# Kernel optimization log

Hardware: AMD Instinct MI355X
Metric: run time of the kernel (lower is better)

## Reference

```python
import jax, jax.numpy as jnp
import numpy as np

D_MODEL = 1024
N_HEADS = 16
D_K = D_MODEL // N_HEADS
D_FF = 4096
EPS = 1e-5


def _layernorm(x, g, b):
    mu = jnp.mean(x, axis=-1, keepdims=True)
    var = jnp.var(x, axis=-1, keepdims=True)
    return (x - mu) * jax.lax.rsqrt(var + EPS) * g + b


def setup_inputs() -> dict:
    key = jax.random.key(0)
    ks = jax.random.split(key, 12)
    s = 0.02
    x = jax.random.normal(ks[0], (2, 2048, D_MODEL), dtype=jnp.float32)
    # Linear weights stored [in, out] so y = x @ W + b
    wq = jax.random.normal(ks[1], (D_MODEL, D_MODEL), dtype=jnp.float32) * s
    wk = jax.random.normal(ks[2], (D_MODEL, D_MODEL), dtype=jnp.float32) * s
    wv = jax.random.normal(ks[3], (D_MODEL, D_MODEL), dtype=jnp.float32) * s
    wo = jax.random.normal(ks[4], (D_MODEL, D_MODEL), dtype=jnp.float32) * s
    bq = jnp.zeros((D_MODEL,), jnp.float32)
    bk = jnp.zeros((D_MODEL,), jnp.float32)
    bv = jnp.zeros((D_MODEL,), jnp.float32)
    bo = jnp.zeros((D_MODEL,), jnp.float32)
    ln1_g = jnp.ones((D_MODEL,), jnp.float32)
    ln1_b = jnp.zeros((D_MODEL,), jnp.float32)
    ln2_g = jnp.ones((D_MODEL,), jnp.float32)
    ln2_b = jnp.zeros((D_MODEL,), jnp.float32)
    w1 = jax.random.normal(ks[5], (D_MODEL, D_FF), dtype=jnp.float32) * s
    b1 = jnp.zeros((D_FF,), jnp.float32)
    w2 = jax.random.normal(ks[6], (D_FF, D_MODEL), dtype=jnp.float32) * s
    b2 = jnp.zeros((D_MODEL,), jnp.float32)
    return {"x": x, "wq": wq, "bq": bq, "wk": wk, "bk": bk, "wv": wv, "bv": bv,
            "wo": wo, "bo": bo, "ln1_g": ln1_g, "ln1_b": ln1_b,
            "ln2_g": ln2_g, "ln2_b": ln2_b, "w1": w1, "b1": b1, "w2": w2, "b2": b2}


def reference(x, wq, bq, wk, bk, wv, bv, wo, bo, ln1_g, ln1_b, ln2_g, ln2_b, w1, b1, w2, b2):
    B, S, _ = x.shape
    res = x
    # project and split heads: [B, S, H, Dk]
    q = (x @ wq + bq).reshape(B, S, N_HEADS, D_K)
    k = (x @ wk + bk).reshape(B, S, N_HEADS, D_K)
    v = (x @ wv + bv).reshape(B, S, N_HEADS, D_K)
    # full score matrix [B, H, Sq, Sk] (faithful to unfused original)
    scores = jnp.einsum('bqhd,bkhd->bhqk', q, k) / jnp.sqrt(jnp.float32(D_K))
    weights = jax.nn.softmax(scores, axis=-1)
    attn = jnp.einsum('bhqk,bkhd->bqhd', weights, v).reshape(B, S, D_MODEL)
    x = _layernorm(res + attn @ wo + bo, ln1_g, ln1_b)
    res = x
    h = jax.nn.relu(x @ w1 + b1)
    x = _layernorm(res + h @ w2 + b2, ln2_g, ln2_b)
    return x
```

## Files before the change

kernel.cpp:

```cpp
#include <hip/hip_runtime.h>
#include <hip/hip_bf16.h>
#include <stdint.h>


typedef __hip_bfloat16 bf16;
typedef short bf16x8 __attribute__((ext_vector_type(8)));
typedef float f32x4 __attribute__((ext_vector_type(4)));

__device__ __forceinline__ float bf2f_lo(unsigned u) { return __uint_as_float(u << 16); }
__device__ __forceinline__ float bf2f_hi(unsigned u) { return __uint_as_float(u & 0xffff0000u); }
__device__ __forceinline__ ushort f2bf(float f) {
  union { bf16 h; ushort u; } c; c.h = __float2bfloat16(f); return c.u;
}
__device__ __forceinline__ bool is_f32(const uint* probe) { return probe[0] == 0x3F800000u; }
__device__ __forceinline__ float ld_param(const void* p, size_t i, bool f32) {
  return f32 ? ((const float*)p)[i] : __bfloat162float(((const bf16*)p)[i]);
}

template <bool A_EXT, bool RES_EXT>
__device__ __forceinline__ void gemm_body(
    const void* __restrict__ Av, const ushort* __restrict__ BT,
    const void* __restrict__ bias, const void* __restrict__ res,
    void* __restrict__ C, int N_, int K_, int bm, int bn,
    int kb, int ke, int mode, const uint* probe) {
  __shared__ ushort Asm_[128 * 32];
  __shared__ ushort Bsm_[128 * 32];

  const bool F32 = is_f32(probe);
  const bool AF = A_EXT && F32;

  const int tid = threadIdx.x;
  const int wave = tid >> 6;
  const int lane = tid & 63;
  const int wm = wave & 1, wn = wave >> 1;

  const int r0 = tid >> 2;
  const int c0 = (tid & 3) * 8;
  const int dA0 = r0 * 32 + c0;
  const int dA1 = dA0 + 64 * 32;

  const size_t aRow0 = (size_t)(bm * 128 + r0) * K_;
  const size_t aRow1 = aRow0 + (size_t)64 * K_;
  const ushort* pB0 = BT + (size_t)(bn * 128 + r0) * K_ + c0;
  const ushort* pB1 = pB0 + (size_t)64 * K_;

  auto ld4 = [&](int kk, uint4& A0, uint4& A1, uint4& B0, uint4& B1) {
    if (AF) {
      const float* Af = (const float*)Av;
      const float4 f0 = *(const float4*)(Af + aRow0 + kk + c0);
      const float4 f1 = *(const float4*)(Af + aRow0 + kk + c0 + 4);
      const float4 g0 = *(const float4*)(Af + aRow1 + kk + c0);
      const float4 g1 = *(const float4*)(Af + aRow1 + kk + c0 + 4);
      A0.x = (uint)f2bf(f0.x) | ((uint)f2bf(f0.y) << 16);
      A0.y = (uint)f2bf(f0.z) | ((uint)f2bf(f0.w) << 16);
      A0.z = (uint)f2bf(f1.x) | ((uint)f2bf(f1.y) << 16);
      A0.w = (uint)f2bf(f1.z) | ((uint)f2bf(f1.w) << 16);
      A1.x = (uint)f2bf(g0.x) | ((uint)f2bf(g0.y) << 16);
      A1.y = (uint)f2bf(g0.z) | ((uint)f2bf(g0.w) << 16);
      A1.z = (uint)f2bf(g1.x) | ((uint)f2bf(g1.y) << 16);
      A1.w = (uint)f2bf(g1.z) | ((uint)f2bf(g1.w) << 16);
    } else {
      const ushort* Ab = (const ushort*)Av;
      A0 = *(const uint4*)(Ab + aRow0 + kk + c0);
      A1 = *(const uint4*)(Ab + aRow1 + kk + c0);
    }
    B0 = *(const uint4*)(pB0 + kk);
    B1 = *(const uint4*)(pB1 + kk);
  };

  f32x4 zero = {0.f, 0.f, 0.f, 0.f};
  f32x4 acc[4][4];
#pragma unroll
  for (int i = 0; i < 4; ++i)
#pragma unroll
    for (int j = 0; j < 4; ++j) acc[i][j] = zero;

  const int m16 = lane & 15;
  const int quad = lane >> 4;
  const int koff = quad * 8;

  uint4 a0, a1, b0, b1;
  ld4(kb, a0, a1, b0, b1);

  for (int k0 = kb; k0 < ke; k0 += 32) {
    __syncthreads();
    *(uint4*)&Asm_[dA0] = a0;
    *(uint4*)&Asm_[dA1] = a1;
    *(uint4*)&Bsm_[dA0] = b0;
    *(uint4*)&Bsm_[dA1] = b1;
    __syncthreads();

    if (k0 + 32 < ke) ld4(k0 + 32, a0, a1, b0, b1);

    bf16x8 af[4], bfr[4];
#pragma unroll
    for (int i = 0; i < 4; ++i)
      af[i] = *(const bf16x8*)&Asm_[(wm * 64 + i * 16 + m16) * 32 + koff];
#pragma unroll
    for (int j = 0; j < 4; ++j)
      bfr[j] = *(const bf16x8*)&Bsm_[(wn * 64 + j * 16 + m16) * 32 + koff];
#pragma unroll
    for (int i = 0; i < 4; ++i)
#pragma unroll
      for (int j = 0; j < 4; ++j)
        acc[i][j] = __builtin_amdgcn_mfma_f32_16x16x32_bf16(af[i], bfr[j], acc[i][j], 0, 0, 0);
  }

  const int row0 = bm * 128 + wm * 64;
  const int col0 = bn * 128 + wn * 64;
#pragma unroll
  for (int j = 0; j < 4; ++j) {
    const int col = col0 + j * 16 + m16;
    const float bv = (mode == 3) ? 0.f : ld_param(bias, col, F32);
#pragma unroll
    for (int i = 0; i < 4; ++i) {
#pragma unroll
      for (int r = 0; r < 4; ++r) {
        const int row = row0 + i * 16 + quad * 4 + r;
        float v = acc[i][j][r] + bv;
        if (mode == 1) v = fmaxf(v, 0.f);
        if (mode == 2) v += ld_param(res, (size_t)row * N_ + col, RES_EXT && F32);
        if (mode >= 2) ((float*)C)[(size_t)row * N_ + col] = v;
        else ((bf16*)C)[(size_t)row * N_ + col] = __float2bfloat16(v);
      }
    }
  }
}

__global__ __launch_bounds__(256) void gemm_qkv(
    const void* A, const ushort* BT0, const ushort* BT1, const ushort* BT2,
    const void* b0, const void* b1, const void* b2,
    bf16* C0, bf16* C1, bf16* C2, const uint* probe) {
  const int sel = blockIdx.y >> 3, bn = blockIdx.y & 7;
  const ushort* BT = sel == 0 ? BT0 : (sel == 1 ? BT1 : BT2);
  const void* bb = sel == 0 ? b0 : (sel == 1 ? b1 : b2);
  bf16* C = sel == 0 ? C0 : (sel == 1 ? C1 : C2);
  gemm_body<true, false>(A, BT, bb, nullptr, C, 1024, 1024, blockIdx.x, bn,
                         0, 1024, 0, probe);
}
__global__ __launch_bounds__(256) void gemm_wo_sk(
    const ushort* A, const ushort* BT, const void* bias, const void* res,
    float* C0, float* C1, const uint* probe) {
  const int kz = blockIdx.z;
  gemm_body<false, true>(A, BT, bias, res, kz ? C1 : C0, 1024, 1024,
                         blockIdx.x, blockIdx.y, kz * 512, kz * 512 + 512,
                         kz ? 3 : 2, probe);
}
__global__ __launch_bounds__(256) void gemm_ffn1(
    const ushort* A, const ushort* BT, const void* bias, bf16* C, const uint* probe) {
  gemm_body<false, false>(A, BT, bias, nullptr, C, 4096, 1024,
                          blockIdx.x, blockIdx.y, 0, 1024, 1, probe);
}
__global__ __launch_bounds__(256) void gemm_ffn2_sk(
    const ushort* A, const ushort* BT, const void* bias, const ushort* res,
    float* C0, float* C1, const uint* probe) {
  const int kz = blockIdx.z;
  gemm_body<false, false>(A, BT, bias, res, kz ? C1 : C0, 1024, 4096,
                          blockIdx.x, blockIdx.y, kz * 2048, kz * 2048 + 2048,
                          kz ? 3 : 2, probe);
}

__global__ __launch_bounds__(256) void transpose_all(
    const void* W0, const void* W1, const void* W2, const void* W3,
    const void* W4, const void* W5,
    ushort* D0, ushort* D1, ushort* D2, ushort* D3, ushort* D4, ushort* D5,
    const uint* probe) {
  const int z = blockIdx.z;
  if (z < 4 && blockIdx.x >= 32) return;
  int n0, k0, K_, N_;
  const void* W;
  ushort* D;
  if (z < 4) {
    n0 = blockIdx.x * 32; k0 = blockIdx.y * 32; K_ = 1024; N_ = 1024;
    W = z == 0 ? W0 : z == 1 ? W1 : z == 2 ? W2 : W3;
    D = z == 0 ? D0 : z == 1 ? D1 : z == 2 ? D2 : D3;
  } else if (z == 4) {
    n0 = blockIdx.x * 32; k0 = blockIdx.y * 32; K_ = 1024; N_ = 4096; W = W4; D = D4;
  } else {
    n0 = blockIdx.y * 32; k0 = blockIdx.x * 32; K_ = 4096; N_ = 1024; W = W5; D = D5;
  }
  const bool F32 = is_f32(probe);
  __shared__ ushort tile[32][33];
  const int tx = threadIdx.x & 31, ty = threadIdx.x >> 5;
#pragma unroll
  for (int i = 0; i < 32; i += 8) {
    const size_t src = (size_t)(k0 + ty + i) * N_ + n0 + tx;
    tile[ty + i][tx] = F32 ? f2bf(((const float*)W)[src]) : ((const ushort*)W)[src];
  }
  __syncthreads();
#pragma unroll
  for (int i = 0; i < 32; i += 8)
    D[(size_t)(n0 + ty + i) * K_ + k0 + tx] = tile[tx][ty + i];
}

template <bool OUT_EXT>
__global__ __launch_bounds__(256) void ln_kernel(
    const float* __restrict__ X, const float* __restrict__ P,
    const void* __restrict__ g, const void* __restrict__ bta,
    void* __restrict__ out, const uint* probe) {
  const bool F32 = is_f32(probe);
  const int row = blockIdx.x;
  const int tid = threadIdx.x;
  const float4 a = *(const float4*)(X + (size_t)row * 1024 + tid * 4);
  const float4 b = *(const float4*)(P + (size_t)row * 1024 + tid * 4);
  const float xv[4] = {a.x + b.x, a.y + b.y, a.z + b.z, a.w + b.w};
  float s = xv[0] + xv[1] + xv[2] + xv[3];
  float ss = xv[0] * xv[0] + xv[1] * xv[1] + xv[2] * xv[2] + xv[3] * xv[3];
#pragma unroll
  for (int o = 32; o > 0; o >>= 1) { s += __shfl_down(s, o); ss += __shfl_down(ss, o); }
  __shared__ float red[8];
  if ((tid & 63) == 0) { red[tid >> 6] = s; red[4 + (tid >> 6)] = ss; }
  __syncthreads();
  s = red[0] + red[1] + red[2] + red[3];
  ss = red[4] + red[5] + red[6] + red[7];
  const float mu = s * (1.f / 1024.f);
  const float rstd = rsqrtf(ss * (1.f / 1024.f) - mu * mu + 1e-5f);
#pragma unroll
  for (int i = 0; i < 4; ++i) {
    const size_t idx = (size_t)row * 1024 + tid * 4 + i;
    const float y = (xv[i] - mu) * rstd * ld_param(g, tid * 4 + i, F32) +
                    ld_param(bta, tid * 4 + i, F32);
    if (OUT_EXT && F32) ((float*)out)[idx] = y;
    else ((bf16*)out)[idx] = __float2bfloat16(y);
  }
}

__global__ __launch_bounds__(256) void attn_mfma(
    const ushort* __restrict__ Qm, const ushort* __restrict__ Km,
    const ushort* __restrict__ Vm, ushort* __restrict__ Om) {
  __shared__ ushort Ks[64 * 72];
  __shared__ ushort Vt[64 * 72];
  __shared__ ushort Pw[4][32 * 72];

  const int tid = threadIdx.x;
  const int wave = tid >> 6, lane = tid & 63;
  const int m16 = lane & 15, quad = lane >> 4;
  const int bb = blockIdx.z, h = blockIdx.y;
  const size_t hb = ((size_t)bb * 2048) * 1024 + h * 64;
  const int q0 = blockIdx.x * 128 + wave * 32;

  bf16x8 qf[2][2];
#pragma unroll
  for (int i = 0; i < 2; ++i)
#pragma unroll
    for (int c = 0; c < 2; ++c) {
      const uint4 u = *(const uint4*)(Qm + hb + (size_t)(q0 + 16 * i + m16) * 1024 + c * 32 + quad * 8);
      const uint w[4] = {u.x, u.y, u.z, u.w};
      bf16x8 f;
#pragma unroll
      for (int j = 0; j < 4; ++j) {
        f[2 * j]     = (short)f2bf(bf2f_lo(w[j]) * 0.125f);
        f[2 * j + 1] = (short)f2bf(bf2f_hi(w[j]) * 0.125f);
      }
      qf[i][c] = f;
    }

  f32x4 zero = {0.f, 0.f, 0.f, 0.f};
  f32x4 acc[2][4];
#pragma unroll
  for (int i = 0; i < 2; ++i)
#pragma unroll
    for (int j = 0; j < 4; ++j) acc[i][j] = zero;
  float lp[2][4] = {{0.f, 0.f, 0.f, 0.f}, {0.f, 0.f, 0.f, 0.f}};

  const int skey = tid >> 2;
  const int sd = (tid & 3) * 8;
  const int pp = tid & 31;
  const int dc = tid >> 5;
  const int ka_ = 16 * ((2 * pp) & 3) + ((2 * pp) >> 2);
  const int kb_ = 16 * ((2 * pp + 1) & 3) + ((2 * pp + 1) >> 2);
  const ushort* Kg = Km + hb;
  const ushort* Vg = Vm + hb;

  uint4 kr0, kr1, vr0, vr1;
  kr0 = *(const uint4*)(Kg + (size_t)skey * 1024 + sd);
  kr1 = *(const uint4*)(Kg + (size_t)skey * 1024 + sd + 32);
  vr0 = *(const uint4*)(Vg + (size_t)ka_ * 1024 + dc * 8);
  vr1 = *(const uint4*)(Vg + (size_t)kb_ * 1024 + dc * 8);

  for (int kt = 0; kt < 2048; kt += 64) {
    __syncthreads();
    *(uint4*)&Ks[skey * 72 + sd] = kr0;
    *(uint4*)&Ks[skey * 72 + sd + 32] = kr1;
    {
      const uint va[4] = {vr0.x, vr0.y, vr0.z, vr0.w};
      const uint vb[4] = {vr1.x, vr1.y, vr1.z, vr1.w};
#pragma unroll
      for (int j = 0; j < 8; ++j) {
        const uint lo = (j & 1) ? (va[j >> 1] >> 16) : (va[j >> 1] & 0xffffu);
        const uint hi = (j & 1) ? (vb[j >> 1] & 0xffff0000u) : (vb[j >> 1] << 16);
        *(uint*)&Vt[(dc * 8 + j) * 72 + 2 * pp] = lo | hi;
      }
    }
    __syncthreads();

    if (kt + 64 < 2048) {
      kr0 = *(const uint4*)(Kg + (size_t)(kt + 64 + skey) * 1024 + sd);
      kr1 = *(const uint4*)(Kg + (size_t)(kt + 64 + skey) * 1024 + sd + 32);
      vr0 = *(const uint4*)(Vg + (size_t)(kt + 64 + ka_) * 1024 + dc * 8);
      vr1 = *(const uint4*)(Vg + (size_t)(kt + 64 + kb_) * 1024 + dc * 8);
    }

    f32x4 s[2][4];
#pragma unroll
    for (int i = 0; i < 2; ++i)
#pragma unroll
      for (int jn = 0; jn < 4; ++jn) s[i][jn] = zero;
#pragma unroll
    for (int c = 0; c < 2; ++c) {
      bf16x8 kb4[4];
#pragma unroll
      for (int jn = 0; jn < 4; ++jn)
        kb4[jn] = *(const bf16x8*)&Ks[(jn * 16 + m16) * 72 + c * 32 + quad * 8];
#pragma unroll
      for (int i = 0; i < 2; ++i)
#pragma unroll
        for (int jn = 0; jn < 4; ++jn)
          s[i][jn] = __builtin_amdgcn_mfma_f32_16x16x32_bf16(qf[i][c], kb4[jn], s[i][jn], 0, 0, 0);
    }

#pragma unroll
    for (int i = 0; i < 2; ++i)
#pragma unroll
      for (int r = 0; r < 4; ++r) {
        const float p0 = __expf(s[i][0][r]);
        const float p1 = __expf(s[i][1][r]);
        const float p2 = __expf(s[i][2][r]);
        const float p3 = __expf(s[i][3][r]);
        lp[i][r] += (p0 + p1) + (p2 + p3);
        uint2 pk;
        pk.x = (uint)f2bf(p0) | ((uint)f2bf(p1) << 16);
        pk.y = (uint)f2bf(p2) | ((uint)f2bf(p3) << 16);
        *(uint2*)&Pw[wave][(16 * i + quad * 4 + r) * 72 + m16 * 4] = pk;
      }
    asm volatile("s_waitcnt lgkmcnt(0)" ::: "memory");

#pragma unroll
    for (int c = 0; c < 2; ++c) {
      bf16x8 pa[2], vb4[4];
#pragma unroll
      for (int i = 0; i < 2; ++i)
        pa[i] = *(const bf16x8*)&Pw[wave][(16 * i + m16) * 72 + c * 32 + quad * 8];
#pragma unroll
      for (int jd = 0; jd < 4; ++jd)
        vb4[jd] = *(const bf16x8*)&Vt[(jd * 16 + m16) * 72 + c * 32 + quad * 8];
#pragma unroll
      for (int i = 0; i < 2; ++i)
#pragma unroll
        for (int jd = 0; jd < 4; ++jd)
          acc[i][jd] = __builtin_amdgcn_mfma_f32_16x16x32_bf16(pa[i], vb4[jd], acc[i][jd], 0, 0, 0);
    }
  }

#pragma unroll
  for (int i = 0; i < 2; ++i)
#pragma unroll
    for (int r = 0; r < 4; ++r) {
      float l = lp[i][r];
      l += __shfl_xor(l, 1); l += __shfl_xor(l, 2);
      l += __shfl_xor(l, 4); l += __shfl_xor(l, 8);
      const float inv = 1.f / l;
      const size_t rowoff = hb + (size_t)(q0 + 16 * i + quad * 4 + r) * 1024;
#pragma unroll
      for (int jd = 0; jd < 4; ++jd)
        Om[rowoff + jd * 16 + m16] = f2bf(acc[i][jd][r] * inv);
    }
}

extern "C" void kernel_launch(void* const* d_in, const int* in_sizes, int n_in,
                              void* d_out, int out_size, void* d_ws, size_t ws_size,
                              hipStream_t stream) {
  const void* x   = d_in[0];
  const void* wq  = d_in[1];
  const void* bq  = d_in[2];
  const void* wk  = d_in[3];
  const void* bk  = d_in[4];
  const void* wv  = d_in[5];
  const void* bv  = d_in[6];
  const void* wo  = d_in[7];
  const void* bo  = d_in[8];
  const uint* probe = (const uint*)d_in[9];
  const void* ln1g = d_in[9];
  const void* ln1b = d_in[10];
  const void* ln2g = d_in[11];
  const void* ln2b = d_in[12];
  const void* w1  = d_in[13];
  const void* b1  = d_in[14];
  const void* w2  = d_in[15];
  const void* b2  = d_in[16];

  char* ws = (char*)d_ws;
  const size_t MB = 1ull << 20;
  ushort* wqT = (ushort*)(ws + 0 * MB);
  ushort* wkT = (ushort*)(ws + 2 * MB);
  ushort* wvT = (ushort*)(ws + 4 * MB);
  ushort* woT = (ushort*)(ws + 6 * MB);
  ushort* w1T = (ushort*)(ws + 8 * MB);
  ushort* w2T = (ushort*)(ws + 16 * MB);
  ushort* Qb  = (ushort*)(ws + 24 * MB);
  ushort* Kb  = (ushort*)(ws + 32 * MB);
  ushort* Vb  = (ushort*)(ws + 40 * MB);
  ushort* AO  = (ushort*)(ws + 72 * MB);
  float*  T1  = (float*)(ws + 24 * MB);
  float*  P1w = (float*)(ws + 40 * MB);
  ushort* X1  = (ushort*)(ws + 56 * MB);
  ushort* Hb  = (ushort*)(ws + 24 * MB);
  float*  T1b = (float*)(ws + 0 * MB);
  float*  P1b = (float*)(ws + 64 * MB);

  const dim3 blk(256);
  transpose_all<<<dim3(128, 32, 6), blk, 0, stream>>>(
      wq, wk, wv, wo, w1, w2, wqT, wkT, wvT, woT, w1T, w2T, probe);

  gemm_qkv<<<dim3(32, 24), blk, 0, stream>>>(x, wqT, wkT, wvT, bq, bk, bv,
                                             (bf16*)Qb, (bf16*)Kb, (bf16*)Vb, probe);
  attn_mfma<<<dim3(16, 16, 2), blk, 0, stream>>>(Qb, Kb, Vb, AO);
  gemm_wo_sk<<<dim3(32, 8, 2), blk, 0, stream>>>(AO, woT, bo, x, T1, P1w, probe);
  ln_kernel<false><<<dim3(4096), blk, 0, stream>>>(T1, P1w, ln1g, ln1b, X1, probe);
  gemm_ffn1<<<dim3(32, 32), blk, 0, stream>>>(X1, w1T, b1, (bf16*)Hb, probe);
  gemm_ffn2_sk<<<dim3(32, 8, 2), blk, 0, stream>>>(Hb, w2T, b2, X1, T1b, P1b, probe);
  ln_kernel<true><<<dim3(4096), blk, 0, stream>>>(T1b, P1b, ln2g, ln2b, d_out, probe);
}
```

Measured before the change: 400.3 us.

## Load GEMM tiles directly into LDS and use exp2 with packed bf16 conversions

The GEMM tile loads for bf16 operands now use global_load_lds to copy straight from global memory into shared memory, removing the register staging. The f32-A path still converts A in registers but loads B directly into LDS. This drops the software prefetch of the next tile, so global latency is no longer overlapped with MFMA work. The attention kernel folds log2(e) into the Q scale and uses the hardware exp2, and both kernels use packed float2-to-bf16 conversion to cut VALU work.

```diff
diff --git a/kernel.cpp b/kernel.cpp
--- a/kernel.cpp
+++ b/kernel.cpp
@@ -6,15 +6,31 @@
 typedef __hip_bfloat16 bf16;
 typedef short bf16x8 __attribute__((ext_vector_type(8)));
 typedef float f32x4 __attribute__((ext_vector_type(4)));
+
+#if __has_builtin(__builtin_amdgcn_exp2f)
+#define EXP2F(x) __builtin_amdgcn_exp2f(x)
+#else
+#define EXP2F(x) exp2f(x)
+#endif
 
 __device__ __forceinline__ float bf2f_lo(unsigned u) { return __uint_as_float(u << 16); }
 __device__ __forceinline__ float bf2f_hi(unsigned u) { return __uint_as_float(u & 0xffff0000u); }
 __device__ __forceinline__ ushort f2bf(float f) {
   union { bf16 h; ushort u; } c; c.h = __float2bfloat16(f); return c.u;
 }
+__device__ __forceinline__ uint pk_bf16(float a, float b) {
+  union { __hip_bfloat162 h2; uint u; } c;
+  c.h2 = __float22bfloat162_rn(make_float2(a, b));
+  return c.u;
+}
 __device__ __forceinline__ bool is_f32(const uint* probe) { return probe[0] == 0x3F800000u; }
 __device__ __forceinline__ float ld_param(const void* p, size_t i, bool f32) {
   return f32 ? ((const float*)p)[i] : __bfloat162float(((const bf16*)p)[i]);
+}
+__device__ __forceinline__ void load_lds16(const void* g, void* l) {
+  __builtin_amdgcn_global_load_lds(
+      (const __attribute__((address_space(1))) void*)g,
+      (__attribute__((address_space(3))) void*)l, 16, 0, 0);
 }
 
 template <bool A_EXT, bool RES_EXT>
@@ -44,29 +60,10 @@
   const ushort* pB0 = BT + (size_t)(bn * 128 + r0) * K_ + c0;
   const ushort* pB1 = pB0 + (size_t)64 * K_;
 
-  auto ld4 = [&](int kk, uint4& A0, uint4& A1, uint4& B0, uint4& B1) {
-    if (AF) {
-      const float* Af = (const float*)Av;
-      const float4 f0 = *(const float4*)(Af + aRow0 + kk + c0);
-      const float4 f1 = *(const float4*)(Af + aRow0 + kk + c0 + 4);
-      const float4 g0 = *(const float4*)(Af + aRow1 + kk + c0);
-      const float4 g1 = *(const float4*)(Af + aRow1 + kk + c0 + 4);
-      A0.x = (uint)f2bf(f0.x) | ((uint)f2bf(f0.y) << 16);
-      A0.y = (uint)f2bf(f0.z) | ((uint)f2bf(f0.w) << 16);
-      A0.z = (uint)f2bf(f1.x) | ((uint)f2bf(f1.y) << 16);
-      A0.w = (uint)f2bf(f1.z) | ((uint)f2bf(f1.w) << 16);
-      A1.x = (uint)f2bf(g0.x) | ((uint)f2bf(g0.y) << 16);
-      A1.y = (uint)f2bf(g0.z) | ((uint)f2bf(g0.w) << 16);
-      A1.z = (uint)f2bf(g1.x) | ((uint)f2bf(g1.y) << 16);
-      A1.w = (uint)f2bf(g1.z) | ((uint)f2bf(g1.w) << 16);
-    } else {
-      const ushort* Ab = (const ushort*)Av;
-      A0 = *(const uint4*)(Ab + aRow0 + kk + c0);
-      A1 = *(const uint4*)(Ab + aRow1 + kk + c0);
-    }
-    B0 = *(const uint4*)(pB0 + kk);
-    B1 = *(const uint4*)(pB1 + kk);
-  };
+  char* ABase0 = (char*)Asm_ + wave * 1024;
+  char* ABase1 = ABase0 + 4096;
+  char* BBase0 = (char*)Bsm_ + wave * 1024;
+  char* BBase1 = BBase0 + 4096;
 
   f32x4 zero = {0.f, 0.f, 0.f, 0.f};
   f32x4 acc[4][4];
@@ -79,31 +76,68 @@
   const int quad = lane >> 4;
   const int koff = quad * 8;
 
-  uint4 a0, a1, b0, b1;
-  ld4(kb, a0, a1, b0, b1);
-
-  for (int k0 = kb; k0 < ke; k0 += 32) {
-    __syncthreads();
-    *(uint4*)&Asm_[dA0] = a0;
-    *(uint4*)&Asm_[dA1] = a1;
-    *(uint4*)&Bsm_[dA0] = b0;
-    *(uint4*)&Bsm_[dA1] = b1;
-    __syncthreads();
-
-    if (k0 + 32 < ke) ld4(k0 + 32, a0, a1, b0, b1);
-
-    bf16x8 af[4], bfr[4];
-#pragma unroll
-    for (int i = 0; i < 4; ++i)
-      af[i] = *(const bf16x8*)&Asm_[(wm * 64 + i * 16 + m16) * 32 + koff];
-#pragma unroll
-    for (int j = 0; j < 4; ++j)
-      bfr[j] = *(const bf16x8*)&Bsm_[(wn * 64 + j * 16 + m16) * 32 + koff];
-#pragma unroll
-    for (int i = 0; i < 4; ++i)
+  auto ldA_f32 = [&](int kk, uint4& A0, uint4& A1) {
+    const float* Af = (const float*)Av;
+    const float4 f0 = *(const float4*)(Af + aRow0 + kk + c0);
+    const float4 f1 = *(const float4*)(Af + aRow0 + kk + c0 + 4);
+    const float4 g0 = *(const float4*)(Af + aRow1 + kk + c0);
+    const float4 g1 = *(const float4*)(Af + aRow1 + kk + c0 + 4);
+    A0.x = pk_bf16(f0.x, f0.y); A0.y = pk_bf16(f0.z, f0.w);
+    A0.z = pk_bf16(f1.x, f1.y); A0.w = pk_bf16(f1.z, f1.w);
+    A1.x = pk_bf16(g0.x, g0.y); A1.y = pk_bf16(g0.z, g0.w);
+    A1.z = pk_bf16(g1.x, g1.y); A1.w = pk_bf16(g1.z, g1.w);
+  };
+
+  if (AF) {
+    uint4 a0, a1;
+    ldA_f32(kb, a0, a1);
+    for (int k0 = kb; k0 < ke; k0 += 32) {
+      __syncthreads();
+      *(uint4*)&Asm_[dA0] = a0;
+      *(uint4*)&Asm_[dA1] = a1;
+      load_lds16(pB0 + k0, BBase0);
+      load_lds16(pB1 + k0, BBase1);
+      __syncthreads();
+      if (k0 + 32 < ke) ldA_f32(k0 + 32, a0, a1);
+
+      bf16x8 af[4], bfr[4];
+#pragma unroll
+      for (int i = 0; i < 4; ++i)
+        af[i] = *(const bf16x8*)&Asm_[(wm * 64 + i * 16 + m16) * 32 + koff];
 #pragma unroll
       for (int j = 0; j < 4; ++j)
-        acc[i][j] = __builtin_amdgcn_mfma_f32_16x16x32_bf16(af[i], bfr[j], acc[i][j], 0, 0, 0);
+        bfr[j] = *(const bf16x8*)&Bsm_[(wn * 64 + j * 16 + m16) * 32 + koff];
+#pragma unroll
+      for (int i = 0; i < 4; ++i)
+#pragma unroll
+        for (int j = 0; j < 4; ++j)
+          acc[i][j] = __builtin_amdgcn_mfma_f32_16x16x32_bf16(af[i], bfr[j], acc[i][j], 0, 0, 0);
+    }
+  } else {
+    const ushort* Ab = (const ushort*)Av;
+    const ushort* pA0 = Ab + aRow0 + c0;
+    const ushort* pA1 = Ab + aRow1 + c0;
+    for (int k0 = kb; k0 < ke; k0 += 32) {
+      __syncthreads();
+      load_lds16(pA0 + k0, ABase0);
+      load_lds16(pA1 + k0, ABase1);
+      load_lds16(pB0 + k0, BBase0);
+      load_lds16(pB1 + k0, BBase1);
+      __syncthreads();
+
+      bf16x8 af[4], bfr[4];
+#pragma unroll
+      for (int i = 0; i < 4; ++i)
+        af[i] = *(const bf16x8*)&Asm_[(wm * 64 + i * 16 + m16) * 32 + koff];
+#pragma unroll
+      for (int j = 0; j < 4; ++j)
+        bfr[j] = *(const bf16x8*)&Bsm_[(wn * 64 + j * 16 + m16) * 32 + koff];
+#pragma unroll
+      for (int i = 0; i < 4; ++i)
+#pragma unroll
+        for (int j = 0; j < 4; ++j)
+          acc[i][j] = __builtin_amdgcn_mfma_f32_16x16x32_bf16(af[i], bfr[j], acc[i][j], 0, 0, 0);
+    }
   }
 
   const int row0 = bm * 128 + wm * 64;
@@ -239,6 +273,7 @@
   const size_t hb = ((size_t)bb * 2048) * 1024 + h * 64;
   const int q0 = blockIdx.x * 128 + wave * 32;
 
+  const float QS = 0.125f * 1.44269504f;
   bf16x8 qf[2][2];
 #pragma unroll
   for (int i = 0; i < 2; ++i)
@@ -249,8 +284,9 @@
       bf16x8 f;
 #pragma unroll
       for (int j = 0; j < 4; ++j) {
-        f[2 * j]     = (short)f2bf(bf2f_lo(w[j]) * 0.125f);
-        f[2 * j + 1] = (short)f2bf(bf2f_hi(w[j]) * 0.125f);
+        const uint p = pk_bf16(bf2f_lo(w[j]) * QS, bf2f_hi(w[j]) * QS);
+        f[2 * j]     = (short)(p & 0xffffu);
+        f[2 * j + 1] = (short)(p >> 16);
       }
       qf[i][c] = f;
     }
@@ -323,14 +359,14 @@
     for (int i = 0; i < 2; ++i)
 #pragma unroll
       for (int r = 0; r < 4; ++r) {
-        const float p0 = __expf(s[i][0][r]);
-        const float p1 = __expf(s[i][1][r]);
-        const float p2 = __expf(s[i][2][r]);
-        const float p3 = __expf(s[i][3][r]);
+        const float p0 = EXP2F(s[i][0][r]);
+        const float p1 = EXP2F(s[i][1][r]);
+        const float p2 = EXP2F(s[i][2][r]);
+        const float p3 = EXP2F(s[i][3][r]);
         lp[i][r] += (p0 + p1) + (p2 + p3);
         uint2 pk;
-        pk.x = (uint)f2bf(p0) | ((uint)f2bf(p1) << 16);
-        pk.y = (uint)f2bf(p2) | ((uint)f2bf(p3) << 16);
+        pk.x = pk_bf16(p0, p1);
+        pk.y = pk_bf16(p2, p3);
         *(uint2*)&Pw[wave][(16 * i + quad * 4 + r) * 72 + m16 * 4] = pk;
       }
     asm volatile("s_waitcnt lgkmcnt(0)" ::: "memory");
```

Result: slower. 437.4 us (+9.3%).
